# Optimization experiments

Hardware: AMD Instinct MI355X
Metric: run time of the kernel (lower is better)

The kernel has to match this reference:

```python
import jax, jax.numpy as jnp
import numpy as np

B, T, HID = 2, 2048, 1024
H, HKV, D = 16, 4, 64          # query heads, kv heads, head dim
GLR = 16                        # gate low-rank dim
GATE_LOGIT_NORMALIZER = 16.0
EPS = 1e-6


def setup_inputs() -> dict:
    key = jax.random.key(0)
    ks = jax.random.split(key, 8)
    w = lambda k, shape: jax.random.normal(k, shape, jnp.float32) * 0.02
    return dict(
        hidden_states=jax.random.normal(ks[0], (B, T, HID), jnp.float32),
        Wq=w(ks[1], (HID, H * D)),
        Wk=w(ks[2], (HID, HKV * D)),
        Wv=w(ks[3], (HID, HKV * D)),
        Wo=w(ks[4], (H * D, HID)),
        Wg1=w(ks[5], (HID, GLR)),
        Wg2=w(ks[6], (GLR, HKV * D)),
        bg2=jnp.zeros((HKV * D,), jnp.float32),
        g_norm_weight=jnp.ones((D,), jnp.float32),
    )


def _gla(q, k, v, g):
    """Gated linear attention recurrence.
    q,k,v,g: [B,H,T,D]. State S: [B,H,D,Dv].
    S_t = exp(g_t)[:,None]*S_{t-1} + k_t (outer) v_t ; o_t = (q_t*scale) @ S_t.
    Equivalent math to chunk_gla / fused_recurrent_gla (default scale=D**-0.5).
    """
    scale = q.shape[-1] ** -0.5
    qs = jnp.moveaxis(q * scale, 2, 0)   # [T,B,H,D]
    ks_ = jnp.moveaxis(k, 2, 0)
    vs = jnp.moveaxis(v, 2, 0)
    gs = jnp.moveaxis(g, 2, 0)
    S0 = jnp.zeros(q.shape[:2] + (q.shape[-1], v.shape[-1]), q.dtype)

    def step(S, inp):
        qt, kt, vt, gt = inp
        S = jnp.exp(gt)[..., None] * S + kt[..., None] * vt[..., None, :]
        o = jnp.einsum('bhk,bhkv->bhv', qt, S)
        return S, o

    S, o = jax.lax.scan(step, S0, (qs, ks_, vs, gs))
    return jnp.moveaxis(o, 0, 2), S      # [B,H,T,Dv]


def reference(hidden_states, Wq, Wk, Wv, Wo, Wg1, Wg2, bg2, g_norm_weight):
    b, t, _ = hidden_states.shape
    split = lambda x, h: jnp.transpose(x.reshape(b, t, h, D), (0, 2, 1, 3))  # [B,h,T,D]
    # projections + relu feature map on q,k
    q = jax.nn.relu(split(hidden_states @ Wq, H))
    k = jax.nn.relu(split(hidden_states @ Wk, HKV))
    v = split(hidden_states @ Wv, HKV)
    # low-rank gate -> logsigmoid / normalizer (log-space decay)
    gk = jax.nn.log_sigmoid(split((hidden_states @ Wg1) @ Wg2 + bg2, HKV)) / GATE_LOGIT_NORMALIZER
    # GQA expansion (repeat_interleave over head dim)
    rep = lambda x: jnp.repeat(x, H // HKV, axis=1)
    o, _ = _gla(q, rep(k), rep(v), rep(gk))        # [B,H,T,D]
    o = jnp.transpose(o, (0, 2, 1, 3))              # [B,T,H,D]
    # per-head RMSNorm over head_dim
    var = jnp.mean(jnp.square(o), axis=-1, keepdims=True)
    o = g_norm_weight * (o * jax.lax.rsqrt(var + EPS))
    return o.reshape(b, t, H * D) @ Wo
```

## Files before the change

kernel.cpp:

```cpp
#include <hip/hip_runtime.h>
#include <hip/hip_bf16.h>
#include <math.h>

#define B_    2
#define T_    2048
#define HID_  1024
#define H_    16
#define HKV_  4
#define D_    64
#define GLR_  16
#define NTOK  (B_*T_)
#define KVD   (HKV_*D_)
#define KVSTR 512
#define QD    (H_*D_)
#define NPROJ (QD+KVSTR)
#define CHUNK 64
#define NC    (T_/CHUNK)
#define SCALE 0.125f
#define EPS_  1e-6f

typedef __attribute__((ext_vector_type(8))) short short8;
typedef __attribute__((ext_vector_type(4))) float f32x4;

__device__ __forceinline__ ushort f2b(float f) {
  __hip_bfloat16 h = __float2bfloat16(f);
  return *reinterpret_cast<ushort*>(&h);
}

__device__ __forceinline__ void gload16(const ushort* g, ushort* l) {
  __builtin_amdgcn_global_load_lds(
      (const __attribute__((address_space(1))) unsigned int*)g,
      (__attribute__((address_space(3))) unsigned int*)l, 16, 0, 0);
}

__global__ __launch_bounds__(256) void stage_all(const float* __restrict__ h,
                                                 const float* __restrict__ Wq,
                                                 const float* __restrict__ Wk,
                                                 const float* __restrict__ Wv,
                                                 const float* __restrict__ Wo,
                                                 const float* __restrict__ Wg1,
                                                 ushort* __restrict__ hb,
                                                 ushort* __restrict__ Wqt,
                                                 ushort* __restrict__ Wkvt,
                                                 ushort* __restrict__ Wot,
                                                 ushort* __restrict__ Wg1t) {
  __shared__ ushort tile[64][65];
  int bi = blockIdx.x;
  if (bi < 4096) {
    int i = bi * 256 + threadIdx.x;
    float4 v = *(const float4*)(h + (size_t)i * 4);
    ushort4 o; o.x = f2b(v.x); o.y = f2b(v.y); o.z = f2b(v.z); o.w = f2b(v.w);
    *(ushort4*)(hb + (size_t)i * 4) = o;
    return;
  }
  bi -= 4096;
  if (bi < 64) {
    int idx = bi * 256 + threadIdx.x;
    int kk = idx >> 4, n = idx & 15;
    Wg1t[(size_t)n * HID_ + kk] = f2b(Wg1[(size_t)kk * GLR_ + n]);
    return;
  }
  bi -= 64;
  const float* W; ushort* Wt; int K, N, nb_, kb_;
  if (bi < 256)      { W = Wq; Wt = Wqt;  K = HID_; N = QD;  nb_ = bi & 15; kb_ = bi >> 4; }
  else if (bi < 320) { bi -= 256; W = Wk; Wt = Wkvt; K = HID_; N = KVD; nb_ = bi & 3; kb_ = bi >> 2; }
  else if (bi < 384) { bi -= 320; W = Wv; Wt = Wkvt + (size_t)KVD * HID_; K = HID_; N = KVD; nb_ = bi & 3; kb_ = bi >> 2; }
  else               { bi -= 384; W = Wo; Wt = Wot;  K = QD;  N = HID_; nb_ = bi & 15; kb_ = bi >> 4; }
  int n0 = nb_ * 64, k0 = kb_ * 64;
  for (int idx = threadIdx.x; idx < 64 * 64; idx += 256) {
    int r = idx >> 6, c = idx & 63;
    tile[c][r] = f2b(W[(size_t)(k0 + r) * N + n0 + c]);
  }
  __syncthreads();
  for (int idx = threadIdx.x; idx < 64 * 64; idx += 256) {
    int r = idx >> 6, c = idx & 63;
    Wt[(size_t)(n0 + r) * K + k0 + c] = tile[r][c];
  }
}

__global__ __launch_bounds__(256) void gemm_proj(const ushort* __restrict__ A,
                                                 const ushort* __restrict__ Bt,
                                                 float* __restrict__ q,
                                                 float* __restrict__ kvo) {
  __shared__ ushort As[128][32];
  __shared__ ushort Bs[128][32];
  const int t = threadIdx.x;
  const int rowBase = blockIdx.y * 128, colBase = blockIdx.x * 128;
  const int lane = t & 63, w = t >> 6;
  const int wr = w >> 1, wc = w & 1;
  const int lrow = lane & 15, hi = lane >> 4;
  const int K = HID_;
  f32x4 acc[4][4];
#pragma unroll
  for (int mi = 0; mi < 4; ++mi)
#pragma unroll
    for (int ni = 0; ni < 4; ++ni) acc[mi][ni] = (f32x4){0.f, 0.f, 0.f, 0.f};

  for (int k0 = 0; k0 < K; k0 += 32) {
#pragma unroll
    for (int l = 0; l < 2; ++l) {
      int idx = t + (l << 8);
      int row = idx >> 2, ch = (idx & 3) << 3;
      gload16(&A [(size_t)(rowBase + row) * K + k0 + ch], &As[0][0] + idx * 8);
      gload16(&Bt[(size_t)(colBase + row) * K + k0 + ch], &Bs[0][0] + idx * 8);
    }
    __syncthreads();
    short8 af[4], bf[4];
#pragma unroll
    for (int mi = 0; mi < 4; ++mi)
      af[mi] = *(const short8*)&As[wr * 64 + mi * 16 + lrow][hi * 8];
#pragma unroll
    for (int ni = 0; ni < 4; ++ni)
      bf[ni] = *(const short8*)&Bs[wc * 64 + ni * 16 + lrow][hi * 8];
#pragma unroll
    for (int mi = 0; mi < 4; ++mi)
#pragma unroll
      for (int ni = 0; ni < 4; ++ni)
        acc[mi][ni] = __builtin_amdgcn_mfma_f32_16x16x32_bf16(af[mi], bf[ni], acc[mi][ni], 0, 0, 0);
    __syncthreads();
  }
#pragma unroll
  for (int mi = 0; mi < 4; ++mi)
#pragma unroll
    for (int ni = 0; ni < 4; ++ni)
#pragma unroll
      for (int r = 0; r < 4; ++r) {
        int gm = rowBase + wr * 64 + mi * 16 + hi * 4 + r;
        int gn = colBase + wc * 64 + ni * 16 + lrow;
        float val = acc[mi][ni][r];
        if (gn < QD) q[(size_t)gm * QD + gn] = fmaxf(val, 0.f);
        else         kvo[(size_t)gm * KVSTR + gn - QD] = val;
      }
}

__global__ __launch_bounds__(256) void gemm_bf16_mfma(const ushort* __restrict__ A,
                                                      const ushort* __restrict__ Bt,
                                                      float* __restrict__ C,
                                                      int M, int N, int K) {
  __shared__ ushort As[128][32];
  __shared__ ushort Bs[128][32];
  const int t = threadIdx.x;
  const int rowBase = blockIdx.y * 128, colBase = blockIdx.x * 128;
  const int lane = t & 63, w = t >> 6;
  const int wr = w >> 1, wc = w & 1;
  const int lrow = lane & 15, hi = lane >> 4;
  f32x4 acc[4][4];
#pragma unroll
  for (int mi = 0; mi < 4; ++mi)
#pragma unroll
    for (int ni = 0; ni < 4; ++ni) acc[mi][ni] = (f32x4){0.f, 0.f, 0.f, 0.f};

  for (int k0 = 0; k0 < K; k0 += 32) {
#pragma unroll
    for (int l = 0; l < 2; ++l) {
      int idx = t + (l << 8);
      int row = idx >> 2, ch = (idx & 3) << 3;
      gload16(&A [(size_t)(rowBase + row) * K + k0 + ch], &As[0][0] + idx * 8);
      gload16(&Bt[(size_t)(colBase + row) * K + k0 + ch], &Bs[0][0] + idx * 8);
    }
    __syncthreads();
    short8 af[4], bf[4];
#pragma unroll
    for (int mi = 0; mi < 4; ++mi)
      af[mi] = *(const short8*)&As[wr * 64 + mi * 16 + lrow][hi * 8];
#pragma unroll
    for (int ni = 0; ni < 4; ++ni)
      bf[ni] = *(const short8*)&Bs[wc * 64 + ni * 16 + lrow][hi * 8];
#pragma unroll
    for (int mi = 0; mi < 4; ++mi)
#pragma unroll
      for (int ni = 0; ni < 4; ++ni)
        acc[mi][ni] = __builtin_amdgcn_mfma_f32_16x16x32_bf16(af[mi], bf[ni], acc[mi][ni], 0, 0, 0);
    __syncthreads();
  }
#pragma unroll
  for (int mi = 0; mi < 4; ++mi)
#pragma unroll
    for (int ni = 0; ni < 4; ++ni)
#pragma unroll
      for (int r = 0; r < 4; ++r) {
        int gm = rowBase + wr * 64 + mi * 16 + hi * 4 + r;
        int gn = colBase + wc * 64 + ni * 16 + lrow;
        C[(size_t)gm * N + gn] = acc[mi][ni][r];
      }
}

__global__ __launch_bounds__(256) void gate_cumsum(const ushort* __restrict__ hb,
                                                   const ushort* __restrict__ Wg1t,
                                                   const float* __restrict__ Wg2,
                                                   const float* __restrict__ bg2,
                                                   float* __restrict__ bc) {
  __shared__ float gts[CHUNK][GLR_ + 1];
  const int t = threadIdx.x, lane = t & 63, w = t >> 6;
  const int lrow = lane & 15, hi = lane >> 4;
  const int c0 = blockIdx.x * CHUNK;
  const int b = c0 / T_, tloc = c0 % T_;
  {
    f32x4 acc = (f32x4){0.f, 0.f, 0.f, 0.f};
#pragma unroll
    for (int kk = 0; kk < 32; ++kk) {
      int k0 = kk * 32 + hi * 8;
      short8 a = *(const short8*)&hb[(size_t)(c0 + w * 16 + lrow) * HID_ + k0];
      short8 bf = *(const short8*)&Wg1t[(size_t)lrow * HID_ + k0];
      acc = __builtin_amdgcn_mfma_f32_16x16x32_bf16(a, bf, acc, 0, 0, 0);
    }
#pragma unroll
    for (int r = 0; r < 4; ++r) gts[w * 16 + hi * 4 + r][lrow] = acc[r];
  }
  __syncthreads();
  {
    const int c = t;
    const int j = c >> 6, d = c & 63;
    const int gj = b * HKV_ + j;
    const float bias = bg2[c];
    float run = 0.f;
    size_t base = ((size_t)gj * T_ + tloc) * D_ + d;
    for (int tok = 0; tok < CHUNK; ++tok) {
      float acc2 = bias;
#pragma unroll
      for (int r = 0; r < GLR_; ++r) acc2 += gts[tok][r] * Wg2[r * KVD + c];
      float ls = fminf(acc2, 0.f) - log1pf(expf(-fabsf(acc2)));
      run += ls * (1.0f / 16.0f);
      bc[base + (size_t)tok * D_] = run;
    }
  }
}

__global__ __launch_bounds__(256) void chunk_kv(const float* __restrict__ kv,
                                                const float* __restrict__ bc,
                                                float* __restrict__ Mt,
                                                float* __restrict__ E) {
  __shared__ float ks[CHUNK][D_ + 1];
  __shared__ float vs[CHUNK][D_ + 1];
  __shared__ float blast[D_];
  int blk = blockIdx.x;
  int c = blk % NC, gj = blk / NC;
  int b = gj >> 2, j = gj & 3;
  size_t kb = ((size_t)(b * T_ + c * CHUNK)) * KVSTR + j * D_;
  size_t bb = ((size_t)gj * T_ + c * CHUNK) * D_;
  if (threadIdx.x < D_) blast[threadIdx.x] = bc[bb + (size_t)(CHUNK - 1) * D_ + threadIdx.x];
  __syncthreads();
  for (int idx = threadIdx.x; idx < CHUNK * D_; idx += 256) {
    int t = idx >> 6, col = idx & 63;
    float bv = bc[bb + idx];
    ks[t][col] = fmaxf(kv[kb + (size_t)t * KVSTR + col], 0.f) * expf(blast[col] - bv);
    vs[t][col] = kv[kb + (size_t)t * KVSTR + 256 + col];
  }
  __syncthreads();
  int jv = threadIdx.x >> 2;
  int i0 = (threadIdx.x & 3) * 16;
  float acc[16];
#pragma unroll
  for (int l = 0; l < 16; ++l) acc[l] = 0.f;
  for (int t = 0; t < CHUNK; ++t) {
    float vt_ = vs[t][jv];
#pragma unroll
    for (int l = 0; l < 16; ++l) acc[l] += vt_ * ks[t][i0 + l];
  }
  size_t mbase = (size_t)blk * D_ * D_ + (size_t)jv * D_ + i0;
#pragma unroll
  for (int l = 0; l < 16; ++l) Mt[mbase + l] = acc[l];
  if (threadIdx.x < D_) E[(size_t)blk * D_ + threadIdx.x] = expf(blast[threadIdx.x]);
}

__global__ __launch_bounds__(256) void state_scan(const float* __restrict__ Mt,
                                                  const float* __restrict__ E,
                                                  float* __restrict__ Sbt) {
  int gj = blockIdx.x >> 4;
  int elem = ((blockIdx.x & 15) << 8) + threadIdx.x;
  int i = elem & 63;
  float S = 0.f;
#pragma unroll
  for (int c = 0; c < NC; ++c) {
    size_t base = ((size_t)gj * NC + c) * (D_ * D_) + elem;
    Sbt[base] = S;
    S = E[((size_t)gj * NC + c) * D_ + i] * S + Mt[base];
  }
}

__global__ __launch_bounds__(256) void gla_out(const float* __restrict__ q,
                                               const float* __restrict__ kv,
                                               const float* __restrict__ bc,
                                               const float* __restrict__ Sbt,
                                               const float* __restrict__ gw,
                                               ushort* __restrict__ obh) {
  __shared__ ushort qes[64][72];
  __shared__ ushort kes[64][72];
  __shared__ ushort vts[64][72];
  __shared__ ushort sts[64][72];
  __shared__ ushort Al [64][72];
  int blk = blockIdx.x;
  int c = blk % NC, bh = blk / NC;
  int b = bh / H_, h = bh % H_;
  int j = h >> 2, gj = b * HKV_ + j;
  size_t nb = (size_t)(b * T_ + c * CHUNK);
  size_t bb = ((size_t)gj * T_ + c * CHUNK) * D_;
  size_t sbase = ((size_t)gj * NC + c) * D_ * D_;
  const int t = threadIdx.x, lane = t & 63, w = t >> 6;
  const int lrow = lane & 15, hi = lane >> 4;
  for (int idx = t; idx < CHUNK * D_; idx += 256) {
    int tt = idx >> 6, col = idx & 63;
    float bv = bc[bb + idx];
    qes[tt][col] = f2b(q[(nb + tt) * QD + h * D_ + col] * expf(bv) * SCALE);
    kes[tt][col] = f2b(fmaxf(kv[(nb + tt) * KVSTR + j * D_ + col], 0.f) * expf(-bv));
    vts[col][tt] = f2b(kv[(nb + tt) * KVSTR + 256 + j * D_ + col]);
    sts[tt][col] = f2b(Sbt[sbase + idx]);
  }
  __syncthreads();
  {
    const int ti = w;
#pragma unroll
    for (int si = 0; si < 4; ++si) {
      f32x4 acc = (f32x4){0.f, 0.f, 0.f, 0.f};
      if (si <= ti) {
#pragma unroll
        for (int kk = 0; kk < 2; ++kk) {
          short8 a  = *(const short8*)&qes[ti * 16 + lrow][kk * 32 + hi * 8];
          short8 bf = *(const short8*)&kes[si * 16 + lrow][kk * 32 + hi * 8];
          acc = __builtin_amdgcn_mfma_f32_16x16x32_bf16(a, bf, acc, 0, 0, 0);
        }
      }
#pragma unroll
      for (int r = 0; r < 4; ++r) {
        int grow = ti * 16 + hi * 4 + r, gcol = si * 16 + lrow;
        Al[grow][gcol] = f2b(gcol <= grow ? acc[r] : 0.f);
      }
    }
  }
  __syncthreads();
  {
    float o[4][4];
#pragma unroll
    for (int ni = 0; ni < 4; ++ni) {
      f32x4 acc = (f32x4){0.f, 0.f, 0.f, 0.f};
#pragma unroll
      for (int kk = 0; kk < 2; ++kk) {
        short8 a  = *(const short8*)&qes[w * 16 + lrow][kk * 32 + hi * 8];
        short8 bf = *(const short8*)&sts[ni * 16 + lrow][kk * 32 + hi * 8];
        acc = __builtin_amdgcn_mfma_f32_16x16x32_bf16(a, bf, acc, 0, 0, 0);
      }
#pragma unroll
      for (int kk = 0; kk < 2; ++kk) {
        short8 a  = *(const short8*)&Al[w * 16 + lrow][kk * 32 + hi * 8];
        short8 bf = *(const short8*)&vts[ni * 16 + lrow][kk * 32 + hi * 8];
        acc = __builtin_amdgcn_mfma_f32_16x16x32_bf16(a, bf, acc, 0, 0, 0);
      }
#pragma unroll
      for (int r = 0; r < 4; ++r) o[ni][r] = acc[r];
    }
#pragma unroll
    for (int r = 0; r < 4; ++r) {
      float ss = o[0][r] * o[0][r] + o[1][r] * o[1][r]
               + o[2][r] * o[2][r] + o[3][r] * o[3][r];
      ss += __shfl_xor(ss, 1, 64);
      ss += __shfl_xor(ss, 2, 64);
      ss += __shfl_xor(ss, 4, 64);
      ss += __shfl_xor(ss, 8, 64);
      float inv = rsqrtf(ss * (1.0f / D_) + EPS_);
      size_t rowoff = (nb + w * 16 + hi * 4 + r) * QD + h * D_;
#pragma unroll
      for (int ni = 0; ni < 4; ++ni) {
        int d = ni * 16 + lrow;
        obh[rowoff + d] = f2b(gw[d] * o[ni][r] * inv);
      }
    }
  }
}

extern "C" void kernel_launch(void* const* d_in, const int* in_sizes, int n_in,
                              void* d_out, int out_size, void* d_ws, size_t ws_size,
                              hipStream_t stream) {
  const float* h   = (const float*)d_in[0];
  const float* Wq  = (const float*)d_in[1];
  const float* Wk  = (const float*)d_in[2];
  const float* Wv  = (const float*)d_in[3];
  const float* Wo  = (const float*)d_in[4];
  const float* Wg1 = (const float*)d_in[5];
  const float* Wg2 = (const float*)d_in[6];
  const float* bg2 = (const float*)d_in[7];
  const float* gw  = (const float*)d_in[8];
  float* out = (float*)d_out;

  float* q   = (float*)d_ws;
  float* kv  = q  + (size_t)NTOK * QD;
  float* bc  = kv + (size_t)NTOK * KVSTR;
  float* Sbt = bc + (size_t)B_ * HKV_ * T_ * D_;
  float* Mt  = Sbt + (size_t)B_ * HKV_ * NC * D_ * D_;
  float* E   = Mt + (size_t)B_ * HKV_ * NC * D_ * D_;
  ushort* hb   = (ushort*)(E + (size_t)B_ * HKV_ * NC * D_);
  ushort* Wqt  = hb   + (size_t)NTOK * HID_;
  ushort* Wkvt = Wqt  + (size_t)HID_ * QD;
  ushort* Wot  = Wkvt + (size_t)KVSTR * HID_;
  ushort* Wg1t = Wot  + (size_t)HID_ * QD;
  ushort* obh = hb;

  dim3 blk(256);
  stage_all<<<4800, blk, 0, stream>>>(h, Wq, Wk, Wv, Wo, Wg1, hb, Wqt, Wkvt, Wot, Wg1t);
  gemm_proj<<<dim3(NPROJ / 128, NTOK / 128), blk, 0, stream>>>(hb, Wqt, q, kv);
  gate_cumsum<<<NTOK / CHUNK, blk, 0, stream>>>(hb, Wg1t, Wg2, bg2, bc);
  chunk_kv<<<B_ * HKV_ * NC, blk, 0, stream>>>(kv, bc, Mt, E);
  state_scan<<<B_ * HKV_ * 16, blk, 0, stream>>>(Mt, E, Sbt);
  gla_out<<<B_ * H_ * NC, blk, 0, stream>>>(q, kv, bc, Sbt, gw, obh);
  gemm_bf16_mfma<<<dim3(HID_ / 128, NTOK / 128), blk, 0, stream>>>(obh, Wot, out, NTOK, HID_, HID_);
}
```

Before: 210.6 us.

## Store q/k/v projections in bf16 and use MFMA for chunk KV outer products

The projection GEMM now writes q and kv as bf16 instead of fp32, which halves the intermediate write and read traffic for gla_out and chunk_kv. chunk_kv replaces its scalar FMA loop with bf16 MFMA over transposed k and v tiles in shared memory. The workspace layout is reordered to match. The cost is reduced precision for q, k and v and for the per-chunk state contributions, which may add numerical error.

```diff
diff --git a/kernel.cpp b/kernel.cpp
--- a/kernel.cpp
+++ b/kernel.cpp
@@ -25,6 +25,10 @@
 __device__ __forceinline__ ushort f2b(float f) {
   __hip_bfloat16 h = __float2bfloat16(f);
   return *reinterpret_cast<ushort*>(&h);
+}
+__device__ __forceinline__ float b2f(ushort u) {
+  __hip_bfloat16 h = *reinterpret_cast<__hip_bfloat16*>(&u);
+  return __bfloat162float(h);
 }
 
 __device__ __forceinline__ void gload16(const ushort* g, ushort* l) {
@@ -80,8 +84,8 @@
 
 __global__ __launch_bounds__(256) void gemm_proj(const ushort* __restrict__ A,
                                                  const ushort* __restrict__ Bt,
-                                                 float* __restrict__ q,
-                                                 float* __restrict__ kvo) {
+                                                 ushort* __restrict__ qb,
+                                                 ushort* __restrict__ kvb) {
   __shared__ ushort As[128][32];
   __shared__ ushort Bs[128][32];
   const int t = threadIdx.x;
@@ -128,8 +132,8 @@
         int gm = rowBase + wr * 64 + mi * 16 + hi * 4 + r;
         int gn = colBase + wc * 64 + ni * 16 + lrow;
         float val = acc[mi][ni][r];
-        if (gn < QD) q[(size_t)gm * QD + gn] = fmaxf(val, 0.f);
-        else         kvo[(size_t)gm * KVSTR + gn - QD] = val;
+        if (gn < QD) qb[(size_t)gm * QD + gn] = f2b(fmaxf(val, 0.f));
+        else         kvb[(size_t)gm * KVSTR + gn - QD] = f2b(val);
       }
 }
 
@@ -226,41 +230,43 @@
   }
 }
 
-__global__ __launch_bounds__(256) void chunk_kv(const float* __restrict__ kv,
+__global__ __launch_bounds__(256) void chunk_kv(const ushort* __restrict__ kvb,
                                                 const float* __restrict__ bc,
                                                 float* __restrict__ Mt,
                                                 float* __restrict__ E) {
-  __shared__ float ks[CHUNK][D_ + 1];
-  __shared__ float vs[CHUNK][D_ + 1];
+  __shared__ ushort vts[64][72];
+  __shared__ ushort kts[64][72];
   __shared__ float blast[D_];
   int blk = blockIdx.x;
   int c = blk % NC, gj = blk / NC;
   int b = gj >> 2, j = gj & 3;
   size_t kb = ((size_t)(b * T_ + c * CHUNK)) * KVSTR + j * D_;
   size_t bb = ((size_t)gj * T_ + c * CHUNK) * D_;
-  if (threadIdx.x < D_) blast[threadIdx.x] = bc[bb + (size_t)(CHUNK - 1) * D_ + threadIdx.x];
-  __syncthreads();
-  for (int idx = threadIdx.x; idx < CHUNK * D_; idx += 256) {
-    int t = idx >> 6, col = idx & 63;
+  const int t = threadIdx.x, lane = t & 63, w = t >> 6;
+  const int lrow = lane & 15, hi = lane >> 4;
+  if (t < D_) blast[t] = bc[bb + (size_t)(CHUNK - 1) * D_ + t];
+  __syncthreads();
+  for (int idx = t; idx < CHUNK * D_; idx += 256) {
+    int tt = idx >> 6, col = idx & 63;
     float bv = bc[bb + idx];
-    ks[t][col] = fmaxf(kv[kb + (size_t)t * KVSTR + col], 0.f) * expf(blast[col] - bv);
-    vs[t][col] = kv[kb + (size_t)t * KVSTR + 256 + col];
-  }
-  __syncthreads();
-  int jv = threadIdx.x >> 2;
-  int i0 = (threadIdx.x & 3) * 16;
-  float acc[16];
-#pragma unroll
-  for (int l = 0; l < 16; ++l) acc[l] = 0.f;
-  for (int t = 0; t < CHUNK; ++t) {
-    float vt_ = vs[t][jv];
-#pragma unroll
-    for (int l = 0; l < 16; ++l) acc[l] += vt_ * ks[t][i0 + l];
-  }
-  size_t mbase = (size_t)blk * D_ * D_ + (size_t)jv * D_ + i0;
-#pragma unroll
-  for (int l = 0; l < 16; ++l) Mt[mbase + l] = acc[l];
-  if (threadIdx.x < D_) E[(size_t)blk * D_ + threadIdx.x] = expf(blast[threadIdx.x]);
+    kts[col][tt] = f2b(fmaxf(b2f(kvb[kb + (size_t)tt * KVSTR + col]), 0.f) * expf(blast[col] - bv));
+    vts[col][tt] = kvb[kb + (size_t)tt * KVSTR + 256 + col];
+  }
+  __syncthreads();
+#pragma unroll
+  for (int ni = 0; ni < 4; ++ni) {
+    f32x4 acc = (f32x4){0.f, 0.f, 0.f, 0.f};
+#pragma unroll
+    for (int kk = 0; kk < 2; ++kk) {
+      short8 a  = *(const short8*)&vts[w * 16 + lrow][kk * 32 + hi * 8];
+      short8 bf = *(const short8*)&kts[ni * 16 + lrow][kk * 32 + hi * 8];
+      acc = __builtin_amdgcn_mfma_f32_16x16x32_bf16(a, bf, acc, 0, 0, 0);
+    }
+#pragma unroll
+    for (int r = 0; r < 4; ++r)
+      Mt[(size_t)blk * D_ * D_ + (size_t)(w * 16 + hi * 4 + r) * D_ + ni * 16 + lrow] = acc[r];
+  }
+  if (t < D_) E[(size_t)blk * D_ + t] = expf(blast[t]);
 }
 
 __global__ __launch_bounds__(256) void state_scan(const float* __restrict__ Mt,
@@ -278,8 +284,8 @@
   }
 }
 
-__global__ __launch_bounds__(256) void gla_out(const float* __restrict__ q,
-                                               const float* __restrict__ kv,
+__global__ __launch_bounds__(256) void gla_out(const ushort* __restrict__ qb,
+                                               const ushort* __restrict__ kvb,
                                                const float* __restrict__ bc,
                                                const float* __restrict__ Sbt,
                                                const float* __restrict__ gw,
@@ -301,9 +307,9 @@
   for (int idx = t; idx < CHUNK * D_; idx += 256) {
     int tt = idx >> 6, col = idx & 63;
     float bv = bc[bb + idx];
-    qes[tt][col] = f2b(q[(nb + tt) * QD + h * D_ + col] * expf(bv) * SCALE);
-    kes[tt][col] = f2b(fmaxf(kv[(nb + tt) * KVSTR + j * D_ + col], 0.f) * expf(-bv));
-    vts[col][tt] = f2b(kv[(nb + tt) * KVSTR + 256 + j * D_ + col]);
+    qes[tt][col] = f2b(b2f(qb[(nb + tt) * QD + h * D_ + col]) * expf(bv) * SCALE);
+    kes[tt][col] = f2b(fmaxf(b2f(kvb[(nb + tt) * KVSTR + j * D_ + col]), 0.f) * expf(-bv));
+    vts[col][tt] = kvb[(nb + tt) * KVSTR + 256 + j * D_ + col];
     sts[tt][col] = f2b(Sbt[sbase + idx]);
   }
   __syncthreads();
@@ -381,25 +387,25 @@
   const float* gw  = (const float*)d_in[8];
   float* out = (float*)d_out;
 
-  float* q   = (float*)d_ws;
-  float* kv  = q  + (size_t)NTOK * QD;
-  float* bc  = kv + (size_t)NTOK * KVSTR;
-  float* Sbt = bc + (size_t)B_ * HKV_ * T_ * D_;
-  float* Mt  = Sbt + (size_t)B_ * HKV_ * NC * D_ * D_;
-  float* E   = Mt + (size_t)B_ * HKV_ * NC * D_ * D_;
-  ushort* hb   = (ushort*)(E + (size_t)B_ * HKV_ * NC * D_);
+  ushort* qb   = (ushort*)d_ws;
+  ushort* kvb  = qb   + (size_t)NTOK * QD;
+  ushort* hb   = kvb  + (size_t)NTOK * KVSTR;
   ushort* Wqt  = hb   + (size_t)NTOK * HID_;
   ushort* Wkvt = Wqt  + (size_t)HID_ * QD;
   ushort* Wot  = Wkvt + (size_t)KVSTR * HID_;
   ushort* Wg1t = Wot  + (size_t)HID_ * QD;
+  float* bc  = (float*)(Wg1t + (size_t)GLR_ * HID_);
+  float* Sbt = bc + (size_t)B_ * HKV_ * T_ * D_;
+  float* Mt  = Sbt + (size_t)B_ * HKV_ * NC * D_ * D_;
+  float* E   = Mt + (size_t)B_ * HKV_ * NC * D_ * D_;
   ushort* obh = hb;
 
   dim3 blk(256);
   stage_all<<<4800, blk, 0, stream>>>(h, Wq, Wk, Wv, Wo, Wg1, hb, Wqt, Wkvt, Wot, Wg1t);
-  gemm_proj<<<dim3(NPROJ / 128, NTOK / 128), blk, 0, stream>>>(hb, Wqt, q, kv);
+  gemm_proj<<<dim3(NPROJ / 128, NTOK / 128), blk, 0, stream>>>(hb, Wqt, qb, kvb);
   gate_cumsum<<<NTOK / CHUNK, blk, 0, stream>>>(hb, Wg1t, Wg2, bg2, bc);
-  chunk_kv<<<B_ * HKV_ * NC, blk, 0, stream>>>(kv, bc, Mt, E);
+  chunk_kv<<<B_ * HKV_ * NC, blk, 0, stream>>>(kvb, bc, Mt, E);
   state_scan<<<B_ * HKV_ * 16, blk, 0, stream>>>(Mt, E, Sbt);
-  gla_out<<<B_ * H_ * NC, blk, 0, stream>>>(q, kv, bc, Sbt, gw, obh);
+  gla_out<<<B_ * H_ * NC, blk, 0, stream>>>(qb, kvb, bc, Sbt, gw, obh);
   gemm_bf16_mfma<<<dim3(HID_ / 128, NTOK / 128), blk, 0, stream>>>(obh, Wot, out, NTOK, HID_, HID_);
 }
```

Result: faster. 200.8 us (-4.7%).
